# Kernel tuning notes

Hardware: AMD Instinct MI355X
Metric: run time of the kernel (lower is better)

Reference implementation:

```python
import jax, jax.numpy as jnp
import numpy as np

LATENT = 256
HIDDEN = 512
NODE_F = 128
MAX_NODES = 50
B = 128


def _mk_linear(key, fan_in, fan_out):
    kw, kb = jax.random.split(key)
    bound = 1.0 / np.sqrt(fan_in)
    W = jax.random.uniform(kw, (fan_in, fan_out), jnp.float32, -bound, bound)
    b = jax.random.uniform(kb, (fan_out,), jnp.float32, -bound, bound)
    return W, b


def setup_inputs() -> dict:
    key = jax.random.key(0)
    ks = jax.random.split(key, 7)
    z = jax.random.normal(ks[0], (B, LATENT), jnp.float32)
    # node decoder: latent -> hidden -> hidden -> max_nodes*node_features
    nw1, nb1 = _mk_linear(ks[1], LATENT, HIDDEN)
    nw2, nb2 = _mk_linear(ks[2], HIDDEN, HIDDEN)
    nw3, nb3 = _mk_linear(ks[3], HIDDEN, MAX_NODES * NODE_F)
    # edge decoder: latent + 2*node_features -> hidden -> hidden//2 -> 1
    ew1, eb1 = _mk_linear(ks[4], LATENT + 2 * NODE_F, HIDDEN)
    ew2, eb2 = _mk_linear(ks[5], HIDDEN, HIDDEN // 2)
    ew3, eb3 = _mk_linear(ks[6], HIDDEN // 2, 1)
    return {"z": z,
            "nw1": nw1, "nb1": nb1, "nw2": nw2, "nb2": nb2, "nw3": nw3, "nb3": nb3,
            "ew1": ew1, "eb1": eb1, "ew2": ew2, "eb2": eb2, "ew3": ew3, "eb3": eb3}


def reference(z, nw1, nb1, nw2, nb2, nw3, nb3, ew1, eb1, ew2, eb2, ew3, eb3):
    # ---- node decoder ----
    h = jax.nn.relu(z @ nw1 + nb1)
    h = jax.nn.relu(h @ nw2 + nb2)
    node_logits = h @ nw3 + nb3                      # [B, MAX_NODES*NODE_F]
    node_feats = node_logits.reshape(z.shape[0], MAX_NODES, NODE_F)
    node_probs = jax.nn.sigmoid(node_feats)

    # ---- edge decoder: vectorize the O(N^2) python loop over upper-tri pairs ----
    # jnp.triu_indices matches the torch loop order: i ascending, j ascending per i.
    ii, jj = jnp.triu_indices(MAX_NODES, k=1)        # [P] each, P = 1225
    ni = node_feats[:, ii, :]                        # [B, P, NODE_F]
    nj = node_feats[:, jj, :]                        # [B, P, NODE_F]
    zb = jnp.broadcast_to(z[:, None, :], (z.shape[0], ii.shape[0], z.shape[1]))
    edge_in = jnp.concatenate([zb, ni, nj], axis=-1)  # [B, P, LATENT+2*NODE_F]
    e = jax.nn.relu(edge_in @ ew1 + eb1)             # [B, P, HIDDEN]
    e = jax.nn.relu(e @ ew2 + eb2)                   # [B, P, HIDDEN//2]
    edge_probs = jax.nn.sigmoid(e @ ew3 + eb3)[..., 0]  # [B, P]
    return node_probs, edge_probs
```

## Files before the change

### kernel.cpp

```cpp
#include <hip/hip_runtime.h>
#include <hip/hip_bf16.h>
#include <math.h>

#define LATENT 256
#define HIDDEN 512
#define NODE_F 128
#define MAX_NODES 50
#define NPAIRS 1225
#define BATCH 128
#define NODE_OUT 6400
#define MTILE 64
#define TPB 10
#define NBLK 256

typedef __attribute__((ext_vector_type(8))) short short8;
typedef __attribute__((ext_vector_type(4))) float float4v;

union S8U { short8 s; unsigned int u[4]; };

__device__ __forceinline__ float bf2f(ushort u) {
    union { unsigned int i; float f; } v; v.i = ((unsigned int)u) << 16; return v.f;
}
__device__ __forceinline__ ushort f2bf(float f) {
    union { unsigned int i; float f; } v; v.f = f;
    unsigned int r = v.i + 0x7fffu + ((v.i >> 16) & 1u);
    return (ushort)(r >> 16);
}
__device__ __forceinline__ unsigned int pk_bf16(float f0, float f1) {
    __hip_bfloat162 p = __float22bfloat162_rn(float2{f0, f1});
    unsigned int w; __builtin_memcpy(&w, &p, 4); return w;
}
__device__ __forceinline__ float sigmoidf(float x) {
    return 1.0f / (1.0f + __expf(-x));
}

#define TR3_B0   0
#define EW2_B0   800
#define WIU_B0   832
#define WIV_B0   848
#define ZC_B0    864
#define ND_B0    1120
#define PT_B0    1376
#define PREPK_NB 1381

__global__ __launch_bounds__(256) void k_prep_all(
    const float* __restrict__ nw3, ushort* __restrict__ nw3T,
    const float* __restrict__ ew1, const float* __restrict__ ew2,
    ushort* __restrict__ ew2T, ushort* __restrict__ wijT,
    const float* __restrict__ z, const float* __restrict__ eb1,
    float* __restrict__ Zc,
    const float* __restrict__ nw1, const float* __restrict__ nb1,
    const float* __restrict__ nw2, const float* __restrict__ nb2,
    ushort* __restrict__ h2b, int* __restrict__ ptab)
{
    __shared__ float smem[64 * 65];
    int b = blockIdx.x;
    int tid = threadIdx.x;
    int tx = tid & 63, ty = tid >> 6;

    if (b < EW2_B0) {
        int bb = b - TR3_B0;
        int k0 = (bb & 7) * 64;
        int n0 = (bb >> 3) * 64;
#pragma unroll
        for (int r = 0; r < 16; r++) {
            int row = r * 4 + ty;
            smem[row * 65 + tx] = nw3[(k0 + row) * NODE_OUT + n0 + tx];
        }
        __syncthreads();
#pragma unroll
        for (int c = 0; c < 16; c++) {
            int n = c * 4 + ty;
            nw3T[(size_t)(n0 + n) * HIDDEN + k0 + tx] = f2bf(smem[tx * 65 + n]);
        }
    } else if (b < WIU_B0) {
        int bb = b - EW2_B0;
        int k0 = (bb >> 2) * 64;
        int n0 = (bb & 3) * 64;
#pragma unroll
        for (int r = 0; r < 16; r++) {
            int row = r * 4 + ty;
            smem[row * 65 + tx] = ew2[(k0 + row) * 256 + n0 + tx];
        }
        __syncthreads();
#pragma unroll
        for (int c = 0; c < 16; c++) {
            int n = c * 4 + ty;
            ew2T[(n0 + n) * HIDDEN + k0 + tx] = f2bf(smem[tx * 65 + n]);
        }
    } else if (b < WIV_B0) {
        int bb = b - WIU_B0;
        int k0 = (bb >> 3) * 64;
        int n0 = (bb & 7) * 64;
#pragma unroll
        for (int r = 0; r < 16; r++) {
            int row = r * 4 + ty;
            smem[row * 65 + tx] = ew1[(256 + k0 + row) * 512 + n0 + tx];
        }
        __syncthreads();
#pragma unroll
        for (int c = 0; c < 16; c++) {
            int n = c * 4 + ty;
            wijT[(n0 + n) * NODE_F + k0 + tx] = f2bf(smem[tx * 65 + n]);
        }
    } else if (b < ZC_B0) {
        int bb = b - WIV_B0;
        int k0 = (bb >> 3) * 64;
        int n0 = (bb & 7) * 64;
#pragma unroll
        for (int r = 0; r < 16; r++) {
            int row = r * 4 + ty;
            smem[row * 65 + tx] = ew1[(384 + k0 + row) * 512 + n0 + tx];
        }
        __syncthreads();
#pragma unroll
        for (int c = 0; c < 16; c++) {
            int n = c * 4 + ty;
            wijT[(512 + n0 + n) * NODE_F + k0 + tx] = f2bf(smem[tx * 65 + n]);
        }
    } else if (b < ND_B0) {
        int b2 = b - ZC_B0;
        int r = b2 >> 1, o = (b2 & 1) * 256 + tid;
        float* zs = smem;
        zs[tid] = z[r * LATENT + tid];
        __syncthreads();
        float acc = 0.f;
#pragma unroll 8
        for (int k = 0; k < LATENT; k++) acc += zs[k] * ew1[k * HIDDEN + o];
        Zc[r * HIDDEN + o] = acc + eb1[o];
    } else if (b < PT_B0) {
        int b2 = b - ND_B0;
        int r = b2 >> 1, half = b2 & 1;
        float* zs = smem;
        float* hs = smem + 256;
        zs[tid] = z[r * LATENT + tid];
        __syncthreads();
        float a0 = 0.f, a1 = 0.f;
#pragma unroll 8
        for (int k = 0; k < LATENT; k++) {
            float zk = zs[k];
            a0 += zk * nw1[k * HIDDEN + tid];
            a1 += zk * nw1[k * HIDDEN + tid + 256];
        }
        hs[tid]       = fmaxf(a0 + nb1[tid], 0.f);
        hs[tid + 256] = fmaxf(a1 + nb1[tid + 256], 0.f);
        __syncthreads();
        int o = half * 256 + tid;
        float acc = 0.f;
#pragma unroll 8
        for (int k = 0; k < HIDDEN; k++) acc += hs[k] * nw2[k * HIDDEN + o];
        acc += nb2[o];
        h2b[r * HIDDEN + o] = f2bf(fmaxf(acc, 0.f));
    } else {
        int p = (b - PT_B0) * 256 + tid;
        if (p < NPAIRS) {
            int i = 0, off = 0;
            while (p - off >= MAX_NODES - 1 - i) { off += MAX_NODES - 1 - i; ++i; }
            int j = i + 1 + (p - off);
            ptab[p] = (i << 8) | j;
        }
    }
}

__global__ __launch_bounds__(256, 2) void k_node_uv(
    const ushort* __restrict__ h2b, const ushort* __restrict__ nw3T,
    const float* __restrict__ nb3, const ushort* __restrict__ wijT,
    const float* __restrict__ Zc,
    float* __restrict__ node_probs, ushort* __restrict__ UV)
{
    __shared__ ushort nf_lds[32][132];
    int tid = threadIdx.x;
    int wave = tid >> 6, lane = tid & 63;
    int m16 = lane & 15, quad = lane >> 4;
    int kk0 = quad * 8;

    int nd = blockIdx.x >> 2;
    int m0 = (blockIdx.x & 3) * 32;
    int colbase = nd * 128 + wave * 32;

    float4v acc[2][2];
#pragma unroll
    for (int mf = 0; mf < 2; mf++)
#pragma unroll
        for (int nt = 0; nt < 2; nt++) acc[mf][nt] = (float4v)(0.f);

    const ushort* b0 = nw3T + (size_t)(colbase + m16) * HIDDEN;
    const ushort* b1 = nw3T + (size_t)(colbase + 16 + m16) * HIDDEN;
    const ushort* a0p = h2b + (m0 + m16) * HIDDEN;
    const ushort* a1p = h2b + (m0 + 16 + m16) * HIDDEN;
#pragma unroll
    for (int it = 0; it < 16; ++it) {
        int kk = it * 32 + kk0;
        short8 bf0 = *(const short8*)(b0 + kk);
        short8 bf1 = *(const short8*)(b1 + kk);
        short8 af0 = *(const short8*)(a0p + kk);
        short8 af1 = *(const short8*)(a1p + kk);
        acc[0][0] = __builtin_amdgcn_mfma_f32_16x16x32_bf16(af0, bf0, acc[0][0], 0, 0, 0);
        acc[0][1] = __builtin_amdgcn_mfma_f32_16x16x32_bf16(af0, bf1, acc[0][1], 0, 0, 0);
        acc[1][0] = __builtin_amdgcn_mfma_f32_16x16x32_bf16(af1, bf0, acc[1][0], 0, 0, 0);
        acc[1][1] = __builtin_amdgcn_mfma_f32_16x16x32_bf16(af1, bf1, acc[1][1], 0, 0, 0);
    }
    float bias0 = nb3[colbase + m16];
    float bias1 = nb3[colbase + 16 + m16];
#pragma unroll
    for (int mf = 0; mf < 2; mf++)
#pragma unroll
        for (int nt = 0; nt < 2; nt++) {
            float bias = nt ? bias1 : bias0;
            int colL = wave * 32 + nt * 16 + m16;
#pragma unroll
            for (int t = 0; t < 4; t++) {
                int rowL = mf * 16 + quad * 4 + t;
                float v = acc[mf][nt][t] + bias;
                node_probs[(size_t)(m0 + rowL) * NODE_OUT + nd * 128 + colL] = sigmoidf(v);
                nf_lds[rowL][colL] = f2bf(v);
            }
        }
    __syncthreads();

    short8 Areg[2][4];
#pragma unroll
    for (int mf = 0; mf < 2; mf++)
#pragma unroll
        for (int ks = 0; ks < 4; ks++)
            Areg[mf][ks] = *(const short8*)&nf_lds[mf * 16 + m16][ks * 32 + kk0];

    bool isU = (wave < 2);
#pragma unroll
    for (int nfi = 0; nfi < 16; ++nfi) {
        int colg = wave * 256 + nfi * 16 + m16;
        const ushort* bp = wijT + colg * NODE_F + kk0;
        float4v u0 = (float4v)(0.f), u1 = (float4v)(0.f);
#pragma unroll
        for (int ks = 0; ks < 4; ks++) {
            short8 bfr = *(const short8*)(bp + ks * 32);
            u0 = __builtin_amdgcn_mfma_f32_16x16x32_bf16(Areg[0][ks], bfr, u0, 0, 0, 0);
            u1 = __builtin_amdgcn_mfma_f32_16x16x32_bf16(Areg[1][ks], bfr, u1, 0, 0, 0);
        }
#pragma unroll
        for (int t = 0; t < 4; t++) {
            int r0g = m0 + quad * 4 + t;
            float z0 = 0.f, z1 = 0.f;
            if (isU) {
                z0 = Zc[(size_t)r0g * HIDDEN + colg];
                z1 = Zc[(size_t)(r0g + 16) * HIDDEN + colg];
            }
            UV[(size_t)(r0g * MAX_NODES + nd) * 1024 + colg]        = f2bf(u0[t] + z0);
            UV[(size_t)((r0g + 16) * MAX_NODES + nd) * 1024 + colg] = f2bf(u1[t] + z1);
        }
    }
}

__global__ __launch_bounds__(512, 2) void k_edge8(
    const ushort* __restrict__ UV,
    const ushort* __restrict__ ew2T, const float* __restrict__ ew3,
    const float* __restrict__ eb2, const float* __restrict__ eb3,
    const int* __restrict__ ptab, float* __restrict__ out_edges)
{
    __shared__ __align__(16) ushort h1[2][MTILE][HIDDEN + 8];
    __shared__ float part[2][MTILE][33];
    __shared__ int uo5[TPB][MTILE], vo5[TPB][MTILE];

    int tid  = threadIdx.x;
    int blk  = blockIdx.x;
    int b    = blk >> 1;
    int ti0  = (blk & 1) * TPB;

    if (tid < MTILE) {
#pragma unroll
        for (int t = 0; t < TPB; t++) {
            int p = (ti0 + t) * MTILE + tid;
            if (p >= NPAIRS) p = NPAIRS - 1;
            int ij = ptab[p];
            uo5[t][tid] = (b * MAX_NODES + (ij >> 8)) * 1024;
            vo5[t][tid] = (b * MAX_NODES + (ij & 255)) * 1024 + 512;
        }
    }

    int wave = tid >> 6, lane = tid & 63;
    int m16 = lane & 15, quad = lane >> 4;
    int c8 = lane * 8;
    int kk0 = quad * 8;
    int par = (wave >> 2) & 1;

    const ushort* bb0 = ew2T + (wave * 32 + m16) * HIDDEN;
    const ushort* bb1 = ew2T + (wave * 32 + 16 + m16) * HIDDEN;
    short8 Breg[16][2];
#pragma unroll
    for (int kc = 0; kc < 16; kc++) {
        Breg[kc][0] = *(const short8*)(bb0 + kc * 32 + kk0);
        Breg[kc][1] = *(const short8*)(bb1 + kc * 32 + kk0);
    }
    float eb2v[2], ew3v[2];
    eb2v[0] = eb2[wave * 32 + m16];      eb2v[1] = eb2[wave * 32 + 16 + m16];
    ew3v[0] = ew3[wave * 32 + m16];      ew3v[1] = ew3[wave * 32 + 16 + m16];

    __syncthreads();

#pragma unroll
    for (int rr = 0; rr < 8; rr++) {
        int r = wave * 8 + rr;
        short8 u8 = *(const short8*)(UV + uo5[0][r] + c8);
        short8 v8 = *(const short8*)(UV + vo5[0][r] + c8);
        S8U hh;
#pragma unroll
        for (int e2 = 0; e2 < 4; e2++) {
            float f0 = fmaxf(bf2f((ushort)u8[e2 * 2])     + bf2f((ushort)v8[e2 * 2]), 0.f);
            float f1 = fmaxf(bf2f((ushort)u8[e2 * 2 + 1]) + bf2f((ushort)v8[e2 * 2 + 1]), 0.f);
            hh.u[e2] = pk_bf16(f0, f1);
        }
        *(short8*)&h1[0][r][c8] = hh.s;
    }
    __syncthreads();

    for (int t = 0; t < TPB; t++) {
        int cur = t & 1, nxt = cur ^ 1;
        bool hasNext = (t + 1 < TPB);

        if (t > 0 && tid < MTILE) {
            int p = (ti0 + t - 1) * MTILE + tid;
            if (p < NPAIRS) {
                float v = eb3[0];
#pragma unroll
                for (int w = 0; w < 32; w++) v += part[nxt][tid][w];
                out_edges[b * NPAIRS + p] = sigmoidf(v);
            }
        }

        float4v acc2[4][2];
#pragma unroll
        for (int mt = 0; mt < 4; mt++)
#pragma unroll
            for (int nt = 0; nt < 2; nt++) acc2[mt][nt] = (float4v)(0.f);

        short8 uu[4], vv[4];

        auto LOAD4 = [&](int rbase) {
#pragma unroll
            for (int rr = 0; rr < 4; rr++) {
                int r = wave * 8 + rbase + rr;
                uu[rr] = *(const short8*)(UV + uo5[t + 1][r] + c8);
                vv[rr] = *(const short8*)(UV + vo5[t + 1][r] + c8);
            }
        };
        auto BUILD4 = [&](int rbase) {
#pragma unroll
            for (int rr = 0; rr < 4; rr++) {
                int r = wave * 8 + rbase + rr;
                S8U hh;
#pragma unroll
                for (int e2 = 0; e2 < 4; e2++) {
                    float f0 = fmaxf(bf2f((ushort)uu[rr][e2 * 2])     + bf2f((ushort)vv[rr][e2 * 2]), 0.f);
                    float f1 = fmaxf(bf2f((ushort)uu[rr][e2 * 2 + 1]) + bf2f((ushort)vv[rr][e2 * 2 + 1]), 0.f);
                    hh.u[e2] = pk_bf16(f0, f1);
                }
                *(short8*)&h1[nxt][r][c8] = hh.s;
            }
        };
        auto MFMA8 = [&](int it0) {
            __builtin_amdgcn_s_setprio(1);
#pragma unroll
            for (int it = it0; it < it0 + 8; ++it) {
                int kk = it * 32 + kk0;
                short8 a0 = *(const short8*)&h1[cur][m16][kk];
                short8 a1 = *(const short8*)&h1[cur][16 + m16][kk];
                short8 a2 = *(const short8*)&h1[cur][32 + m16][kk];
                short8 a3 = *(const short8*)&h1[cur][48 + m16][kk];
                acc2[0][0] = __builtin_amdgcn_mfma_f32_16x16x32_bf16(a0, Breg[it][0], acc2[0][0], 0, 0, 0);
                acc2[1][0] = __builtin_amdgcn_mfma_f32_16x16x32_bf16(a1, Breg[it][0], acc2[1][0], 0, 0, 0);
                acc2[2][0] = __builtin_amdgcn_mfma_f32_16x16x32_bf16(a2, Breg[it][0], acc2[2][0], 0, 0, 0);
                acc2[3][0] = __builtin_amdgcn_mfma_f32_16x16x32_bf16(a3, Breg[it][0], acc2[3][0], 0, 0, 0);
                acc2[0][1] = __builtin_amdgcn_mfma_f32_16x16x32_bf16(a0, Breg[it][1], acc2[0][1], 0, 0, 0);
                acc2[1][1] = __builtin_amdgcn_mfma_f32_16x16x32_bf16(a1, Breg[it][1], acc2[1][1], 0, 0, 0);
                acc2[2][1] = __builtin_amdgcn_mfma_f32_16x16x32_bf16(a2, Breg[it][1], acc2[2][1], 0, 0, 0);
                acc2[3][1] = __builtin_amdgcn_mfma_f32_16x16x32_bf16(a3, Breg[it][1], acc2[3][1], 0, 0, 0);
            }
            __builtin_amdgcn_s_setprio(0);
        };

        if (hasNext) LOAD4(0);
        if (par == 0) {
            if (hasNext) { BUILD4(0); LOAD4(4); }
            MFMA8(0);
            if (hasNext) BUILD4(4);
            MFMA8(8);
        } else {
            MFMA8(0);
            if (hasNext) { BUILD4(0); LOAD4(4); }
            MFMA8(8);
            if (hasNext) BUILD4(4);
        }

#pragma unroll
        for (int mt = 0; mt < 4; mt++)
#pragma unroll
            for (int tt = 0; tt < 4; tt++) {
                float s = 0.f;
#pragma unroll
                for (int nt = 0; nt < 2; nt++)
                    s += fmaxf(acc2[mt][nt][tt] + eb2v[nt], 0.f) * ew3v[nt];
                s += __shfl_xor(s, 1);
                s += __shfl_xor(s, 2);
                if ((m16 & 3) == 0)
                    part[cur][mt * 16 + quad * 4 + tt][wave * 4 + (m16 >> 2)] = s;
            }
        __syncthreads();
    }

    if (tid < MTILE) {
        int p = (ti0 + TPB - 1) * MTILE + tid;
        if (p < NPAIRS) {
            float v = eb3[0];
#pragma unroll
            for (int w = 0; w < 32; w++) v += part[(TPB - 1) & 1][tid][w];
            out_edges[b * NPAIRS + p] = sigmoidf(v);
        }
    }
}

extern "C" void kernel_launch(void* const* d_in, const int* in_sizes, int n_in,
                              void* d_out, int out_size, void* d_ws, size_t ws_size,
                              hipStream_t stream) {
    const float* z   = (const float*)d_in[0];
    const float* nw1 = (const float*)d_in[1];
    const float* nb1 = (const float*)d_in[2];
    const float* nw2 = (const float*)d_in[3];
    const float* nb2 = (const float*)d_in[4];
    const float* nw3 = (const float*)d_in[5];
    const float* nb3 = (const float*)d_in[6];
    const float* ew1 = (const float*)d_in[7];
    const float* eb1 = (const float*)d_in[8];
    const float* ew2 = (const float*)d_in[9];
    const float* eb2 = (const float*)d_in[10];
    const float* ew3 = (const float*)d_in[11];
    const float* eb3 = (const float*)d_in[12];

    char* ws = (char*)d_ws;
    int*    ptab = (int*)(ws);
    ushort* h2b  = (ushort*)(ws + 262144);
    ushort* ew2T = (ushort*)(ws + 2031616);
    ushort* wijT = (ushort*)(ws + 2293760);
    ushort* nw3T = (ushort*)(ws + 2555904);
    float*  Zc   = (float*)(ws + 9109504);
    ushort* UV   = (ushort*)(ws + 9371648);

    float* out_nodes = (float*)d_out;
    float* out_edges = out_nodes + BATCH * NODE_OUT;

    k_prep_all<<<PREPK_NB, 256, 0, stream>>>(nw3, nw3T, ew1, ew2, ew2T, wijT,
                                             z, eb1, Zc, nw1, nb1, nw2, nb2,
                                             h2b, ptab);
    k_node_uv<<<200, 256, 0, stream>>>(h2b, nw3T, nb3, wijT, Zc, out_nodes, UV);
    k_edge8<<<NBLK, 512, 0, stream>>>(UV, ew2T, ew3, eb2, eb3, ptab, out_edges);
}
```

Before: 217.3 us.

## Split edge MLP layer-2 columns across 16 waves with 1024-thread blocks

```diff
diff --git a/kernel.cpp b/kernel.cpp
--- a/kernel.cpp
+++ b/kernel.cpp
@@ -251,7 +251,7 @@
     }
 }
 
-__global__ __launch_bounds__(512, 2) void k_edge8(
+__global__ __launch_bounds__(1024, 3) void k_edge8(
     const ushort* __restrict__ UV,
     const ushort* __restrict__ ew2T, const float* __restrict__ ew3,
     const float* __restrict__ eb2, const float* __restrict__ eb3,
@@ -283,23 +283,19 @@
     int kk0 = quad * 8;
     int par = (wave >> 2) & 1;
 
-    const ushort* bb0 = ew2T + (wave * 32 + m16) * HIDDEN;
-    const ushort* bb1 = ew2T + (wave * 32 + 16 + m16) * HIDDEN;
-    short8 Breg[16][2];
-#pragma unroll
-    for (int kc = 0; kc < 16; kc++) {
-        Breg[kc][0] = *(const short8*)(bb0 + kc * 32 + kk0);
-        Breg[kc][1] = *(const short8*)(bb1 + kc * 32 + kk0);
-    }
-    float eb2v[2], ew3v[2];
-    eb2v[0] = eb2[wave * 32 + m16];      eb2v[1] = eb2[wave * 32 + 16 + m16];
-    ew3v[0] = ew3[wave * 32 + m16];      ew3v[1] = ew3[wave * 32 + 16 + m16];
+    const ushort* bb0 = ew2T + (wave * 16 + m16) * HIDDEN;
+    short8 Breg[16];
+#pragma unroll
+    for (int kc = 0; kc < 16; kc++)
+        Breg[kc] = *(const short8*)(bb0 + kc * 32 + kk0);
+    float eb2v = eb2[wave * 16 + m16];
+    float ew3v = ew3[wave * 16 + m16];
 
     __syncthreads();
 
 #pragma unroll
-    for (int rr = 0; rr < 8; rr++) {
-        int r = wave * 8 + rr;
+    for (int rr = 0; rr < 4; rr++) {
+        int r = wave * 4 + rr;
         short8 u8 = *(const short8*)(UV + uo5[0][r] + c8);
         short8 v8 = *(const short8*)(UV + vo5[0][r] + c8);
         S8U hh;
@@ -327,26 +323,24 @@
             }
         }
 
-        float4v acc2[4][2];
-#pragma unroll
-        for (int mt = 0; mt < 4; mt++)
-#pragma unroll
-            for (int nt = 0; nt < 2; nt++) acc2[mt][nt] = (float4v)(0.f);
-
-        short8 uu[4], vv[4];
-
-        auto LOAD4 = [&](int rbase) {
-#pragma unroll
-            for (int rr = 0; rr < 4; rr++) {
-                int r = wave * 8 + rbase + rr;
+        float4v acc2[4];
+#pragma unroll
+        for (int mt = 0; mt < 4; mt++) acc2[mt] = (float4v)(0.f);
+
+        short8 uu[2], vv[2];
+
+        auto LOAD2 = [&](int rbase) {
+#pragma unroll
+            for (int rr = 0; rr < 2; rr++) {
+                int r = wave * 4 + rbase + rr;
                 uu[rr] = *(const short8*)(UV + uo5[t + 1][r] + c8);
                 vv[rr] = *(const short8*)(UV + vo5[t + 1][r] + c8);
             }
         };
-        auto BUILD4 = [&](int rbase) {
-#pragma unroll
-            for (int rr = 0; rr < 4; rr++) {
-                int r = wave * 8 + rbase + rr;
+        auto BUILD2 = [&](int rbase) {
+#pragma unroll
+            for (int rr = 0; rr < 2; rr++) {
+                int r = wave * 4 + rbase + rr;
                 S8U hh;
 #pragma unroll
                 for (int e2 = 0; e2 < 4; e2++) {
@@ -366,43 +360,37 @@
                 short8 a1 = *(const short8*)&h1[cur][16 + m16][kk];
                 short8 a2 = *(const short8*)&h1[cur][32 + m16][kk];
                 short8 a3 = *(const short8*)&h1[cur][48 + m16][kk];
-                acc2[0][0] = __builtin_amdgcn_mfma_f32_16x16x32_bf16(a0, Breg[it][0], acc2[0][0], 0, 0, 0);
-                acc2[1][0] = __builtin_amdgcn_mfma_f32_16x16x32_bf16(a1, Breg[it][0], acc2[1][0], 0, 0, 0);
-                acc2[2][0] = __builtin_amdgcn_mfma_f32_16x16x32_bf16(a2, Breg[it][0], acc2[2][0], 0, 0, 0);
-                acc2[3][0] = __builtin_amdgcn_mfma_f32_16x16x32_bf16(a3, Breg[it][0], acc2[3][0], 0, 0, 0);
-                acc2[0][1] = __builtin_amdgcn_mfma_f32_16x16x32_bf16(a0, Breg[it][1], acc2[0][1], 0, 0, 0);
-                acc2[1][1] = __builtin_amdgcn_mfma_f32_16x16x32_bf16(a1, Breg[it][1], acc2[1][1], 0, 0, 0);
-                acc2[2][1] = __builtin_amdgcn_mfma_f32_16x16x32_bf16(a2, Breg[it][1], acc2[2][1], 0, 0, 0);
-                acc2[3][1] = __builtin_amdgcn_mfma_f32_16x16x32_bf16(a3, Breg[it][1], acc2[3][1], 0, 0, 0);
+                acc2[0] = __builtin_amdgcn_mfma_f32_16x16x32_bf16(a0, Breg[it], acc2[0], 0, 0, 0);
+                acc2[1] = __builtin_amdgcn_mfma_f32_16x16x32_bf16(a1, Breg[it], acc2[1], 0, 0, 0);
+                acc2[2] = __builtin_amdgcn_mfma_f32_16x16x32_bf16(a2, Breg[it], acc2[2], 0, 0, 0);
+                acc2[3] = __builtin_amdgcn_mfma_f32_16x16x32_bf16(a3, Breg[it], acc2[3], 0, 0, 0);
             }
             __builtin_amdgcn_s_setprio(0);
         };
 
-        if (hasNext) LOAD4(0);
+        if (hasNext) LOAD2(0);
         if (par == 0) {
-            if (hasNext) { BUILD4(0); LOAD4(4); }
+            if (hasNext) { BUILD2(0); LOAD2(2); }
             MFMA8(0);
-            if (hasNext) BUILD4(4);
+            if (hasNext) BUILD2(2);
             MFMA8(8);
         } else {
             MFMA8(0);
-            if (hasNext) { BUILD4(0); LOAD4(4); }
+            if (hasNext) { BUILD2(0); LOAD2(2); }
             MFMA8(8);
-            if (hasNext) BUILD4(4);
+            if (hasNext) BUILD2(2);
         }
 
 #pragma unroll
         for (int mt = 0; mt < 4; mt++)
 #pragma unroll
             for (int tt = 0; tt < 4; tt++) {
-                float s = 0.f;
-#pragma unroll
-                for (int nt = 0; nt < 2; nt++)
-                    s += fmaxf(acc2[mt][nt][tt] + eb2v[nt], 0.f) * ew3v[nt];
+                float s = fmaxf(acc2[mt][tt] + eb2v, 0.f) * ew3v;
                 s += __shfl_xor(s, 1);
                 s += __shfl_xor(s, 2);
-                if ((m16 & 3) == 0)
-                    part[cur][mt * 16 + quad * 4 + tt][wave * 4 + (m16 >> 2)] = s;
+                s += __shfl_xor(s, 4);
+                if ((m16 & 7) == 0)
+                    part[cur][mt * 16 + quad * 4 + tt][wave * 2 + (m16 >> 3)] = s;
             }
         __syncthreads();
     }
@@ -451,5 +439,5 @@
                                              z, eb1, Zc, nw1, nb1, nw2, nb2,
                                              h2b, ptab);
     k_node_uv<<<200, 256, 0, stream>>>(h2b, nw3T, nb3, wijT, Zc, out_nodes, UV);
-    k_edge8<<<NBLK, 512, 0, stream>>>(UV, ew2T, ew3, eb2, eb3, ptab, out_edges);
-}
+    k_edge8<<<NBLK, 1024, 0, stream>>>(UV, ew2T, ew3, eb2, eb3, ptab, out_edges);
+}
```

Result: slower. 232.3 us (+6.9%).
